# Kernel tuning notes

Measured on AMD Instinct MI355X. Metric: run time of the kernel, lower is better.

The kernel has to match this reference:

```python
import jax, jax.numpy as jnp
import numpy as np

D = 512      # d_model
H = 8        # num_heads
HD = D // H  # head_dim = 64 (concat makes per-head dim 2*HD=128)
B = 32       # batch*group
T = 512      # time steps


def setup_inputs() -> dict:
    key = jax.random.key(0)
    ks = jax.random.split(key, 18)
    def W(k):
        return jax.random.normal(k, (D, D), dtype=jnp.float32) * 0.02
    inp = {
        "x_face": jax.random.normal(ks[0], (B, T, D), dtype=jnp.float32),
        "x_skeleton": jax.random.normal(ks[1], (B, T, D), dtype=jnp.float32),
        "wq1": W(ks[2]), "bq1": jnp.zeros((D,), jnp.float32),
        "wk1": W(ks[3]), "bk1": jnp.zeros((D,), jnp.float32),
        "wv1": W(ks[4]), "bv1": jnp.zeros((D,), jnp.float32),
        "wq2": W(ks[5]), "bq2": jnp.zeros((D,), jnp.float32),
        "wk2": W(ks[6]), "bk2": jnp.zeros((D,), jnp.float32),
        "wv2": W(ks[7]), "bv2": jnp.zeros((D,), jnp.float32),
        "wo1": W(ks[8]), "bo1": jnp.zeros((D,), jnp.float32),
        "wo2": W(ks[9]), "bo2": jnp.zeros((D,), jnp.float32),
    }
    return inp


def reference(x_face, x_skeleton,
              wq1, bq1, wk1, bk1, wv1, bv1,
              wq2, bq2, wk2, bk2, wv2, bv2,
              wo1, bo1, wo2, bo2):
    Bt, Tt, _ = x_face.shape

    def proj(x, w, b):
        # torch Linear: x @ W^T + b, then 'b t (h d) -> b h t d'
        return (x @ w.T + b).reshape(Bt, Tt, H, HD).transpose(0, 2, 1, 3)

    q = jnp.concatenate([proj(x_face, wq1, bq1), proj(x_skeleton, wq2, bq2)], axis=3)  # [B,H,T,2*HD]
    k = jnp.concatenate([proj(x_face, wk1, bk1), proj(x_skeleton, wk2, bk2)], axis=3)
    v = jnp.concatenate([proj(x_face, wv1, bv1), proj(x_skeleton, wv2, bv2)], axis=3)

    scores = jnp.einsum('bhid,bhjd->bhij', q, k) / (HD ** 0.5)  # scale by head_dim**0.5 as in source
    attn = jax.nn.softmax(scores, axis=-1)                      # dropout = identity (eval mode)
    out = jnp.einsum('bhij,bhjd->bhid', attn, v)                # [B,H,T,2*HD]
    out = out.transpose(0, 2, 1, 3).reshape(Bt, Tt, 2 * D)      # 'b h t d -> b t (h d)'

    x1, x2 = out[..., :D], out[..., D:]
    return (x1 @ wo1.T + bo1, x2 @ wo2.T + bo2)
```

## Files before the change

kernel.cpp:

```cpp
#include <hip/hip_runtime.h>
#include <hip/hip_bf16.h>
#include <stdint.h>

typedef __hip_bfloat16 bf16;
using f32x4 = __attribute__((ext_vector_type(4))) float;
using s16x8 = __attribute__((ext_vector_type(8))) short;

typedef __attribute__((address_space(1))) unsigned int gu32;
typedef __attribute__((address_space(3))) unsigned int lu32;

__device__ __forceinline__ void gll16(const void* g, void* l) {
  __builtin_amdgcn_global_load_lds((const gu32*)g, (lu32*)l, 16, 0, 0);
}

struct ConvJob { const float* src; bf16* dst; int n4; int pad; };
struct ConvParams { ConvJob j[10]; };
struct alignas(8) Bf4 { bf16 v[4]; };

__global__ void convert_kernel(ConvParams p) {
  ConvJob jb = p.j[blockIdx.z];
  int stride = gridDim.x * blockDim.x;
  for (int i = blockIdx.x * blockDim.x + threadIdx.x; i < jb.n4; i += stride) {
    float4 v = ((const float4*)jb.src)[i];
    Bf4 o;
    o.v[0] = __float2bfloat16(v.x);
    o.v[1] = __float2bfloat16(v.y);
    o.v[2] = __float2bfloat16(v.z);
    o.v[3] = __float2bfloat16(v.w);
    ((Bf4*)jb.dst)[i] = o;
  }
}

struct GemmSlice {
  const bf16* A; const bf16* W; const float* bias;
  bf16* dstQ; float* dstF;
  long lda; int dhalf; float scale; int mode;
};
struct GemmParams { GemmSlice s[6]; };

#define STG_A(v, h) do { \
    const bf16* s_ = Ab + (long)((h) * 128) * lda + (v) * 64; \
    bf16* d_ = lds + (((v) & 1) ? 16384 : 0) + (h) * 8192 + tid * 8; \
    gll16(s_, d_); gll16(s_ + 64 * lda, d_ + 4096); \
  } while (0)

#define STG_B(v, h) do { \
    const bf16* s_ = Wb + (long)((h) * 128) * 512 + (v) * 64; \
    bf16* d_ = lds + 32768 + (((v) & 1) ? 16384 : 0) + (h) * 8192 + tid * 8; \
    gll16(s_, d_); gll16(s_ + 64 * 512, d_ + 4096); \
  } while (0)

#define GPHASE(miBase, STAGE_STMT, WAIT_STMT) do { \
    s16x8 af[4][2]; \
    _Pragma("unroll") \
    for (int i_ = 0; i_ < 4; ++i_) { \
      const bf16* rp_ = bA + (((miBase) + i_) * 16 + fr) * 64; \
      af[i_][0] = *(const s16x8*)(rp_ + cs0); \
      af[i_][1] = *(const s16x8*)(rp_ + cs1); \
    } \
    STAGE_STMT; \
    __builtin_amdgcn_s_barrier(); \
    asm volatile("s_waitcnt lgkmcnt(0)" ::: "memory"); \
    __builtin_amdgcn_sched_barrier(0); \
    __builtin_amdgcn_s_setprio(1); \
    _Pragma("unroll") \
    for (int i_ = 0; i_ < 4; ++i_) \
      _Pragma("unroll") \
      for (int nj_ = 0; nj_ < 2; ++nj_) { \
        acc[(miBase) + i_][nj_] = __builtin_amdgcn_mfma_f32_16x16x32_bf16(af[i_][0], bfr[nj_][0], acc[(miBase) + i_][nj_], 0, 0, 0); \
        acc[(miBase) + i_][nj_] = __builtin_amdgcn_mfma_f32_16x16x32_bf16(af[i_][1], bfr[nj_][1], acc[(miBase) + i_][nj_], 0, 0, 0); \
      } \
    __builtin_amdgcn_s_setprio(0); \
    WAIT_STMT; \
    __builtin_amdgcn_s_barrier(); \
  } while (0)

__global__ __launch_bounds__(512, 2) void gemm_kernel(GemmParams p) {
  __shared__ alignas(16) bf16 lds[65536];
  const GemmSlice sl = p.s[blockIdx.z];
  const long lda = sl.lda;
  const int tid = threadIdx.x;
  const int w = tid >> 6, ln = tid & 63;
  const int fr = ln & 15, fq = ln >> 4;
  const int gm0 = blockIdx.x * 256;
  const int gn0 = blockIdx.y * 256;
  const int r0 = tid >> 3;
  const int c0 = ((tid & 7) ^ (r0 & 7)) * 8;
  const bf16* const Ab = sl.A + (long)(gm0 + r0) * lda + c0;
  const bf16* const Wb = sl.W + (long)(gn0 + r0) * 512 + c0;
  const int cs0 = (fq ^ (fr & 7)) * 8;
  const int cs1 = ((4 + fq) ^ (fr & 7)) * 8;

  f32x4 acc[16][2] = {};

  STG_B(0, 0); STG_B(0, 1); STG_A(0, 0);
  __builtin_amdgcn_sched_barrier(0);
  STG_A(0, 1);
  __builtin_amdgcn_sched_barrier(0);
  STG_B(1, 0); STG_B(1, 1); STG_A(1, 0);
  asm volatile("s_waitcnt vmcnt(8)" ::: "memory");
  __builtin_amdgcn_sched_barrier(0);
  __builtin_amdgcn_s_barrier();

#pragma unroll
  for (int u = 0; u < 8; ++u) {
    const bf16* bA = lds + ((u & 1) ? 16384 : 0);
    const bf16* bB = lds + 32768 + ((u & 1) ? 16384 : 0);
    s16x8 bfr[2][2];
#pragma unroll
    for (int nj_ = 0; nj_ < 2; ++nj_) {
      const bf16* rp_ = bB + (w * 32 + nj_ * 16 + fr) * 64;
      bfr[nj_][0] = *(const s16x8*)(rp_ + cs0);
      bfr[nj_][1] = *(const s16x8*)(rp_ + cs1);
    }
    GPHASE(0, { if (u < 7) STG_A(u + 1, 1); }, {});
    GPHASE(4, { if (u < 6) STG_B(u + 2, 0); },
           { if (u <= 5)      { asm volatile("s_waitcnt vmcnt(10)" ::: "memory"); }
             else if (u == 6) { asm volatile("s_waitcnt vmcnt(8)"  ::: "memory"); }
             else             { asm volatile("s_waitcnt vmcnt(0)"  ::: "memory"); }
             __builtin_amdgcn_sched_barrier(0); });
    GPHASE(8, { if (u < 6) STG_B(u + 2, 1); }, {});
    GPHASE(12, { if (u < 6) STG_A(u + 2, 0); },
           { if (u <= 5)      { asm volatile("s_waitcnt vmcnt(8)" ::: "memory"); __builtin_amdgcn_sched_barrier(0); }
             else if (u == 6) { asm volatile("s_waitcnt vmcnt(2)" ::: "memory"); __builtin_amdgcn_sched_barrier(0); } });
  }

  if (sl.mode == 0) {
#pragma unroll
    for (int mi = 0; mi < 16; ++mi)
#pragma unroll
      for (int nj = 0; nj < 2; ++nj) {
        const int col = gn0 + w * 32 + nj * 16 + fr;
        const int h = col >> 6;
        const int dd = (col & 63) + sl.dhalf;
        const float bia = sl.bias[col];
#pragma unroll
        for (int r = 0; r < 4; ++r) {
          const int row = gm0 + mi * 16 + fq * 4 + r;
          const int b = row >> 9, t = row & 511;
          const float v = (acc[mi][nj][r] + bia) * sl.scale;
          sl.dstQ[(((long)(b * 8 + h) * 512 + t) << 7) + dd] = __float2bfloat16(v);
        }
      }
  } else if (sl.mode == 2) {
#pragma unroll
    for (int mi = 0; mi < 16; ++mi)
#pragma unroll
      for (int nj = 0; nj < 2; ++nj) {
        const int col = gn0 + w * 32 + nj * 16 + fr;
        const int h = col >> 6;
        const int dd = (col & 63) + sl.dhalf;
        const float bia = sl.bias[col];
        const int row0 = gm0 + mi * 16 + fq * 4;
        const int b = row0 >> 9, t = row0 & 511;
        Bf4 o;
#pragma unroll
        for (int r = 0; r < 4; ++r) o.v[r] = __float2bfloat16(acc[mi][nj][r] + bia);
        *(Bf4*)(sl.dstQ + (((long)(b * 8 + h) * 128 + dd) << 9) + t) = o;
      }
  } else {
#pragma unroll
    for (int mi = 0; mi < 16; ++mi)
#pragma unroll
      for (int nj = 0; nj < 2; ++nj) {
        const int col = gn0 + w * 32 + nj * 16 + fr;
        const float bia = sl.bias[col];
#pragma unroll
        for (int r = 0; r < 4; ++r) {
          const int row = gm0 + mi * 16 + fq * 4 + r;
          sl.dstF[(long)row * 512 + col] = acc[mi][nj][r] + bia;
        }
      }
  }
}

#define STAGE(kt, bK, bV) do { \
    _Pragma("unroll") \
    for (int p_ = 0; p_ < 4; ++p_) \
      gll16(kgb + (kt) * 8192 + p_ * 2048, (bK) + tid * 8 + p_ * 2048); \
    _Pragma("unroll") \
    for (int p_ = 0; p_ < 4; ++p_) \
      gll16(vgb + (kt) * 64 + p_ * 16384, (bV) + tid * 8 + p_ * 2048); \
  } while (0)

#define COMPUTE(bK, bV) do { \
  f32x4 s2[2][4] = {}; \
  _Pragma("unroll") \
  for (int ks = 0; ks < 4; ++ks) { \
    _Pragma("unroll") \
    for (int ni = 0; ni < 4; ++ni) { \
      const int row_ = ni * 16 + fr; \
      const s16x8 kf = *(const s16x8*)((bK) + row_ * 128 + ((ks * 32 + fq * 8) ^ ((row_ & 7) << 3))); \
      _Pragma("unroll") \
      for (int mi = 0; mi < 2; ++mi) \
        s2[mi][ni] = __builtin_amdgcn_mfma_f32_16x16x32_bf16(qf[mi][ks], kf, s2[mi][ni], 0, 0, 0); \
    } \
  } \
  _Pragma("unroll") \
  for (int mi = 0; mi < 2; ++mi) \
    _Pragma("unroll") \
    for (int r = 0; r < 4; ++r) { \
      float ps = 0.f; \
      _Pragma("unroll") \
      for (int ni = 0; ni < 4; ++ni) { \
        const float pe = __builtin_amdgcn_exp2f(s2[mi][ni][r]); \
        s2[mi][ni][r] = pe; ps += pe; \
      } \
      ps += __shfl_xor(ps, 1); ps += __shfl_xor(ps, 2); \
      ps += __shfl_xor(ps, 4); ps += __shfl_xor(ps, 8); \
      lrow[mi][r] += ps; \
    } \
  _Pragma("unroll") \
  for (int mi = 0; mi < 2; ++mi) \
    _Pragma("unroll") \
    for (int ni = 0; ni < 4; ++ni) \
      _Pragma("unroll") \
      for (int r = 0; r < 4; ++r) { \
        const int rp = mi * 16 + fq * 4 + r; \
        sPw[rp * 64 + ((ni * 16 + fr) ^ ((rp & 7) << 3))] = __float2bfloat16(s2[mi][ni][r]); \
      } \
  _Pragma("unroll") \
  for (int ks = 0; ks < 2; ++ks) { \
    s16x8 pf[2]; \
    _Pragma("unroll") \
    for (int mi = 0; mi < 2; ++mi) { \
      const int row_ = mi * 16 + fr; \
      pf[mi] = *(const s16x8*)(sPw + row_ * 64 + ((ks * 32 + fq * 8) ^ ((row_ & 7) << 3))); \
    } \
    _Pragma("unroll") \
    for (int nj = 0; nj < 8; ++nj) { \
      const int row_ = nj * 16 + fr; \
      const s16x8 vf = *(const s16x8*)((bV) + row_ * 64 + ((ks * 32 + fq * 8) ^ ((row_ & 7) << 3))); \
      _Pragma("unroll") \
      for (int mi = 0; mi < 2; ++mi) \
        o[mi][nj] = __builtin_amdgcn_mfma_f32_16x16x32_bf16(pf[mi], vf, o[mi][nj], 0, 0, 0); \
    } \
  } \
} while (0)

__global__ __launch_bounds__(256, 2) void attn_kernel(const bf16* __restrict__ Q,
                                                      const bf16* __restrict__ K,
                                                      const bf16* __restrict__ Vt,
                                                      bf16* __restrict__ AO) {
  __shared__ alignas(16) bf16 lds[40960];
  bf16* const ldsK0 = lds;
  bf16* const ldsV0 = lds + 8192;
  bf16* const ldsK1 = lds + 16384;
  bf16* const ldsV1 = lds + 24576;
  bf16* const sP    = lds + 32768;
  const int tid = threadIdx.x;
  const int w = tid >> 6, ln = tid & 63;
  const int fr = ln & 15, fq = ln >> 4;
  const int lg = (blockIdx.x & 7) * 128 + (blockIdx.x >> 3);
  const int bh = lg >> 2;
  const int q0 = (lg & 3) * 128;
  const long base = (long)bh << 16;
  bf16* const sPw = sP + w * 2048;

  const int kr0 = tid >> 4, kc = tid & 15;
  const int vr0 = tid >> 3, vc = tid & 7;
  const bf16* const kgb = K + base + kr0 * 128 + ((kc ^ (kr0 & 7)) * 8);
  const bf16* const vgb = Vt + base + (long)vr0 * 512 + ((vc ^ (vr0 & 7)) * 8);

  {
    const bf16* const qgb = Q + base + (long)q0 * 128 + kr0 * 128 + ((kc ^ (kr0 & 7)) * 8);
#pragma unroll
    for (int p = 0; p < 8; ++p)
      gll16(qgb + p * 2048, lds + tid * 8 + p * 2048);
  }
  __syncthreads();
  s16x8 qf[2][4];
#pragma unroll
  for (int mi = 0; mi < 2; ++mi) {
    const int row = w * 32 + mi * 16 + fr;
#pragma unroll
    for (int ks = 0; ks < 4; ++ks)
      qf[mi][ks] = *(const s16x8*)(lds + row * 128 + ((ks * 32 + fq * 8) ^ ((row & 7) << 3)));
  }
  __syncthreads();

  f32x4 o[2][8] = {};
  float lrow[2][4] = {};

  STAGE(0, ldsK0, ldsV0);
  STAGE(1, ldsK1, ldsV1);

  for (int kt = 0; kt < 7; ++kt) {
    const bf16* bK = (kt & 1) ? ldsK1 : ldsK0;
    const bf16* bV = (kt & 1) ? ldsV1 : ldsV0;
    asm volatile("s_waitcnt vmcnt(8)" ::: "memory");
    __builtin_amdgcn_sched_barrier(0);
    __builtin_amdgcn_s_barrier();
    COMPUTE(bK, bV);
    asm volatile("s_waitcnt lgkmcnt(0)" ::: "memory");
    __builtin_amdgcn_sched_barrier(0);
    __builtin_amdgcn_s_barrier();
    if (kt < 6) STAGE(kt + 2, (bf16*)bK, (bf16*)bV);
  }
  asm volatile("s_waitcnt vmcnt(0)" ::: "memory");
  __builtin_amdgcn_sched_barrier(0);
  __builtin_amdgcn_s_barrier();
  COMPUTE(ldsK1, ldsV1);

  const int b = bh >> 3, h = bh & 7;
  float rl[2][4];
#pragma unroll
  for (int mi = 0; mi < 2; ++mi)
#pragma unroll
    for (int r = 0; r < 4; ++r) rl[mi][r] = 1.f / lrow[mi][r];
#pragma unroll
  for (int mi = 0; mi < 2; ++mi)
#pragma unroll
    for (int nj = 0; nj < 8; ++nj) {
      const int col = h * 128 + nj * 16 + fr;
#pragma unroll
      for (int r = 0; r < 4; ++r) {
        const int trow = q0 + w * 32 + mi * 16 + fq * 4 + r;
        AO[((long)(b * 512 + trow) << 10) + col] = __float2bfloat16(o[mi][nj][r] * rl[mi][r]);
      }
    }
}

extern "C" void kernel_launch(void* const* d_in, const int* in_sizes, int n_in,
                              void* d_out, int out_size, void* d_ws, size_t ws_size,
                              hipStream_t stream) {
  const float* xf = (const float*)d_in[0];
  const float* xs = (const float*)d_in[1];
  const float* w_f[8] = { (const float*)d_in[2], (const float*)d_in[4], (const float*)d_in[6],
                          (const float*)d_in[8], (const float*)d_in[10], (const float*)d_in[12],
                          (const float*)d_in[14], (const float*)d_in[16] };

  bf16* ws = (bf16*)d_ws;
  bf16* XF = ws;
  bf16* XS = ws + 8388608;
  bf16* WW = ws + 16777216;
  bf16* Qb = ws + 18874368;
  bf16* Kb = Qb + 16777216;
  bf16* Vb = Kb + 16777216;
  bf16* AO = ws;

  ConvParams cp;
  cp.j[0] = { xf, XF, 2097152, 0 };
  cp.j[1] = { xs, XS, 2097152, 0 };
  for (int i = 0; i < 8; ++i) cp.j[2 + i] = { w_f[i], WW + i * 262144, 65536, 0 };
  convert_kernel<<<dim3(512, 1, 10), 256, 0, stream>>>(cp);

  const float qsc = 0.125f * 1.44269504088896f;
  GemmParams gp;
  gp.s[0] = { XF, WW + 0 * 262144, (const float*)d_in[3],  Qb, nullptr, 512, 0,  qsc, 0 };
  gp.s[1] = { XS, WW + 3 * 262144, (const float*)d_in[9],  Qb, nullptr, 512, 64, qsc, 0 };
  gp.s[2] = { XF, WW + 1 * 262144, (const float*)d_in[5],  Kb, nullptr, 512, 0,  1.f, 0 };
  gp.s[3] = { XS, WW + 4 * 262144, (const float*)d_in[11], Kb, nullptr, 512, 64, 1.f, 0 };
  gp.s[4] = { XF, WW + 2 * 262144, (const float*)d_in[7],  Vb, nullptr, 512, 0,  1.f, 2 };
  gp.s[5] = { XS, WW + 5 * 262144, (const float*)d_in[13], Vb, nullptr, 512, 64, 1.f, 2 };
  gemm_kernel<<<dim3(64, 2, 6), 512, 0, stream>>>(gp);

  attn_kernel<<<dim3(1024), 256, 0, stream>>>(Qb, Kb, Vb, AO);

  float* out = (float*)d_out;
  GemmParams op;
  op.s[0] = { AO,       WW + 6 * 262144, (const float*)d_in[15], nullptr, out,           1024, 0, 1.f, 1 };
  op.s[1] = { AO + 512, WW + 7 * 262144, (const float*)d_in[17], nullptr, out + 8388608, 1024, 0, 1.f, 1 };
  op.s[2] = op.s[0]; op.s[3] = op.s[0]; op.s[4] = op.s[0]; op.s[5] = op.s[0];
  gemm_kernel<<<dim3(64, 2, 2), 512, 0, stream>>>(op);
}
```

Before: 173.3 us.

## Retile GEMM warps as 2x4 grid with half-K LDS sub-tiles

Changes the GEMM warp layout from each warp covering all 256 rows by 32 columns to a 2x4 warp grid where each warp covers 128 rows by 64 columns. The LDS staging is reorganized into 32-wide K halves with a 4-way XOR swizzle, and the phases and vmcnt waits are rescheduled to match. The intent is to cut LDS fragment reads per MFMA, since each A fragment now feeds 4 MFMAs instead of 2, while keeping the same accumulator count. It risks bank conflicts or wait-count mistakes in the reworked pipeline.

```diff
diff --git a/kernel.cpp b/kernel.cpp
--- a/kernel.cpp
+++ b/kernel.cpp
@@ -39,25 +39,27 @@
 struct GemmParams { GemmSlice s[6]; };
 
 #define STG_A(v, h) do { \
-    const bf16* s_ = Ab + (long)((h) * 128) * lda + (v) * 64; \
-    bf16* d_ = lds + (((v) & 1) ? 16384 : 0) + (h) * 8192 + tid * 8; \
-    gll16(s_, d_); gll16(s_ + 64 * lda, d_ + 4096); \
+    const bf16* s_ = Ab + (v) * 64 + (h) * 32; \
+    bf16* d_ = lds + (((v) & 1) << 14) + (h) * 8192 + tid * 8; \
+    gll16(s_, d_); gll16(s_ + (lda << 7), d_ + 4096); \
   } while (0)
 
 #define STG_B(v, h) do { \
-    const bf16* s_ = Wb + (long)((h) * 128) * 512 + (v) * 64; \
-    bf16* d_ = lds + 32768 + (((v) & 1) ? 16384 : 0) + (h) * 8192 + tid * 8; \
-    gll16(s_, d_); gll16(s_ + 64 * 512, d_ + 4096); \
+    const bf16* s_ = Wb + (v) * 64 + (h) * 32; \
+    bf16* d_ = lds + 32768 + (((v) & 1) << 14) + (h) * 8192 + tid * 8; \
+    gll16(s_, d_); gll16(s_ + (512 << 7), d_ + 4096); \
   } while (0)
 
-#define GPHASE(miBase, STAGE_STMT, WAIT_STMT) do { \
-    s16x8 af[4][2]; \
-    _Pragma("unroll") \
-    for (int i_ = 0; i_ < 4; ++i_) { \
-      const bf16* rp_ = bA + (((miBase) + i_) * 16 + fr) * 64; \
-      af[i_][0] = *(const s16x8*)(rp_ + cs0); \
-      af[i_][1] = *(const s16x8*)(rp_ + cs1); \
-    } \
+#define GP(MB, H, RDB, STAGE_STMT, WAIT_STMT) do { \
+    if (RDB) { \
+      _Pragma("unroll") \
+      for (int nj_ = 0; nj_ < 4; ++nj_) \
+        bfr[nj_] = *(const s16x8*)(bB + (H) * 8192 + brow32 + nj_ * 512 + cw); \
+    } \
+    s16x8 af[4]; \
+    _Pragma("unroll") \
+    for (int i_ = 0; i_ < 4; ++i_) \
+      af[i_] = *(const s16x8*)(bA + (H) * 8192 + arow32 + ((MB) + i_) * 512 + cw); \
     STAGE_STMT; \
     __builtin_amdgcn_s_barrier(); \
     asm volatile("s_waitcnt lgkmcnt(0)" ::: "memory"); \
@@ -66,10 +68,8 @@
     _Pragma("unroll") \
     for (int i_ = 0; i_ < 4; ++i_) \
       _Pragma("unroll") \
-      for (int nj_ = 0; nj_ < 2; ++nj_) { \
-        acc[(miBase) + i_][nj_] = __builtin_amdgcn_mfma_f32_16x16x32_bf16(af[i_][0], bfr[nj_][0], acc[(miBase) + i_][nj_], 0, 0, 0); \
-        acc[(miBase) + i_][nj_] = __builtin_amdgcn_mfma_f32_16x16x32_bf16(af[i_][1], bfr[nj_][1], acc[(miBase) + i_][nj_], 0, 0, 0); \
-      } \
+      for (int nj_ = 0; nj_ < 4; ++nj_) \
+        acc[(MB) + i_][nj_] = __builtin_amdgcn_mfma_f32_16x16x32_bf16(af[i_], bfr[nj_], acc[(MB) + i_][nj_], 0, 0, 0); \
     __builtin_amdgcn_s_setprio(0); \
     WAIT_STMT; \
     __builtin_amdgcn_s_barrier(); \
@@ -82,61 +82,54 @@
   const int tid = threadIdx.x;
   const int w = tid >> 6, ln = tid & 63;
   const int fr = ln & 15, fq = ln >> 4;
+  const int wm = w >> 2, wn = w & 3;
   const int gm0 = blockIdx.x * 256;
   const int gn0 = blockIdx.y * 256;
-  const int r0 = tid >> 3;
-  const int c0 = ((tid & 7) ^ (r0 & 7)) * 8;
+  const int r0 = tid >> 2;
+  const int c0 = ((tid & 3) ^ (r0 & 3)) * 8;
   const bf16* const Ab = sl.A + (long)(gm0 + r0) * lda + c0;
   const bf16* const Wb = sl.W + (long)(gn0 + r0) * 512 + c0;
-  const int cs0 = (fq ^ (fr & 7)) * 8;
-  const int cs1 = ((4 + fq) ^ (fr & 7)) * 8;
-
-  f32x4 acc[16][2] = {};
-
-  STG_B(0, 0); STG_B(0, 1); STG_A(0, 0);
+  const int cw = (fq ^ (fr & 3)) * 8;
+  const int arow32 = (wm * 128 + fr) * 32;
+  const int brow32 = (wn * 64 + fr) * 32;
+
+  f32x4 acc[8][4] = {};
+
+  STG_B(0, 0); STG_A(0, 0); STG_B(0, 1); STG_A(0, 1);
   __builtin_amdgcn_sched_barrier(0);
-  STG_A(0, 1);
-  __builtin_amdgcn_sched_barrier(0);
-  STG_B(1, 0); STG_B(1, 1); STG_A(1, 0);
+  STG_B(1, 0); STG_A(1, 0); STG_B(1, 1);
   asm volatile("s_waitcnt vmcnt(8)" ::: "memory");
   __builtin_amdgcn_sched_barrier(0);
   __builtin_amdgcn_s_barrier();
 
 #pragma unroll
   for (int u = 0; u < 8; ++u) {
-    const bf16* bA = lds + ((u & 1) ? 16384 : 0);
-    const bf16* bB = lds + 32768 + ((u & 1) ? 16384 : 0);
-    s16x8 bfr[2][2];
-#pragma unroll
-    for (int nj_ = 0; nj_ < 2; ++nj_) {
-      const bf16* rp_ = bB + (w * 32 + nj_ * 16 + fr) * 64;
-      bfr[nj_][0] = *(const s16x8*)(rp_ + cs0);
-      bfr[nj_][1] = *(const s16x8*)(rp_ + cs1);
-    }
-    GPHASE(0, { if (u < 7) STG_A(u + 1, 1); }, {});
-    GPHASE(4, { if (u < 6) STG_B(u + 2, 0); },
-           { if (u <= 5)      { asm volatile("s_waitcnt vmcnt(10)" ::: "memory"); }
-             else if (u == 6) { asm volatile("s_waitcnt vmcnt(8)"  ::: "memory"); }
-             else             { asm volatile("s_waitcnt vmcnt(0)"  ::: "memory"); }
-             __builtin_amdgcn_sched_barrier(0); });
-    GPHASE(8, { if (u < 6) STG_B(u + 2, 1); }, {});
-    GPHASE(12, { if (u < 6) STG_A(u + 2, 0); },
-           { if (u <= 5)      { asm volatile("s_waitcnt vmcnt(8)" ::: "memory"); __builtin_amdgcn_sched_barrier(0); }
-             else if (u == 6) { asm volatile("s_waitcnt vmcnt(2)" ::: "memory"); __builtin_amdgcn_sched_barrier(0); } });
+    const bf16* bA = lds + ((u & 1) << 14);
+    const bf16* bB = lds + 32768 + ((u & 1) << 14);
+    s16x8 bfr[4];
+    GP(0, 0, 1, { if (u <= 6) STG_A(u + 1, 1); }, {});
+    GP(4, 0, 0, { if (u <= 5) STG_B(u + 2, 0); },
+       { if (u <= 6) { asm volatile("s_waitcnt vmcnt(6)" ::: "memory"); }
+         else        { asm volatile("s_waitcnt vmcnt(0)" ::: "memory"); }
+         __builtin_amdgcn_sched_barrier(0); });
+    GP(0, 1, 1, { if (u <= 5) STG_A(u + 2, 0); }, {});
+    GP(4, 1, 0, { if (u <= 5) STG_B(u + 2, 1); },
+       { if (u <= 5)      { asm volatile("s_waitcnt vmcnt(8)" ::: "memory"); __builtin_amdgcn_sched_barrier(0); }
+         else if (u == 6) { asm volatile("s_waitcnt vmcnt(2)" ::: "memory"); __builtin_amdgcn_sched_barrier(0); } });
   }
 
   if (sl.mode == 0) {
 #pragma unroll
-    for (int mi = 0; mi < 16; ++mi)
-#pragma unroll
-      for (int nj = 0; nj < 2; ++nj) {
-        const int col = gn0 + w * 32 + nj * 16 + fr;
+    for (int mi = 0; mi < 8; ++mi)
+#pragma unroll
+      for (int nj = 0; nj < 4; ++nj) {
+        const int col = gn0 + wn * 64 + nj * 16 + fr;
         const int h = col >> 6;
         const int dd = (col & 63) + sl.dhalf;
         const float bia = sl.bias[col];
 #pragma unroll
         for (int r = 0; r < 4; ++r) {
-          const int row = gm0 + mi * 16 + fq * 4 + r;
+          const int row = gm0 + wm * 128 + mi * 16 + fq * 4 + r;
           const int b = row >> 9, t = row & 511;
           const float v = (acc[mi][nj][r] + bia) * sl.scale;
           sl.dstQ[(((long)(b * 8 + h) * 512 + t) << 7) + dd] = __float2bfloat16(v);
@@ -144,14 +137,14 @@
       }
   } else if (sl.mode == 2) {
 #pragma unroll
-    for (int mi = 0; mi < 16; ++mi)
-#pragma unroll
-      for (int nj = 0; nj < 2; ++nj) {
-        const int col = gn0 + w * 32 + nj * 16 + fr;
+    for (int mi = 0; mi < 8; ++mi)
+#pragma unroll
+      for (int nj = 0; nj < 4; ++nj) {
+        const int col = gn0 + wn * 64 + nj * 16 + fr;
         const int h = col >> 6;
         const int dd = (col & 63) + sl.dhalf;
         const float bia = sl.bias[col];
-        const int row0 = gm0 + mi * 16 + fq * 4;
+        const int row0 = gm0 + wm * 128 + mi * 16 + fq * 4;
         const int b = row0 >> 9, t = row0 & 511;
         Bf4 o;
 #pragma unroll
@@ -160,14 +153,14 @@
       }
   } else {
 #pragma unroll
-    for (int mi = 0; mi < 16; ++mi)
-#pragma unroll
-      for (int nj = 0; nj < 2; ++nj) {
-        const int col = gn0 + w * 32 + nj * 16 + fr;
+    for (int mi = 0; mi < 8; ++mi)
+#pragma unroll
+      for (int nj = 0; nj < 4; ++nj) {
+        const int col = gn0 + wn * 64 + nj * 16 + fr;
         const float bia = sl.bias[col];
 #pragma unroll
         for (int r = 0; r < 4; ++r) {
-          const int row = gm0 + mi * 16 + fq * 4 + r;
+          const int row = gm0 + wm * 128 + mi * 16 + fq * 4 + r;
           sl.dstF[(long)row * 512 + col] = acc[mi][nj][r] + bia;
         }
       }
```

Result: slower. 179.1 us (+3.3%).
